# Kernel optimization log

Measured on AMD Instinct MI355X. Metric: run time of the kernel, lower is better.

## Reference

```python
import jax, jax.numpy as jnp
import numpy as np

IN_FEATURES = 4096
OUT_FEATURES = 11008
BATCH = 256


def unpack_i4(q):
    # q: [K//2, N] packed bytes; row 2k = low nibble, row 2k+1 = high nibble
    low = q & 15
    high = (q >> 4) & 15
    # interleave -> [K, N]
    return jnp.stack([low, high], axis=1).reshape(q.shape[0] * 2, q.shape[1])


def setup_inputs() -> dict:
    key = jax.random.key(0)
    k1, k2, k3, k4 = jax.random.split(key, 4)
    x = jax.random.normal(k1, (BATCH, IN_FEATURES), dtype=jnp.float32)
    qweight = jax.random.randint(k2, (IN_FEATURES // 2, OUT_FEATURES), 0, 256, dtype=jnp.int32)
    scales = jax.random.uniform(k3, (OUT_FEATURES,), dtype=jnp.float32)
    zeroes = jax.random.normal(k4, (OUT_FEATURES,), dtype=jnp.float32)
    return {"x": x, "qweight": qweight, "scales": scales, "zeroes": zeroes}


def reference(x, qweight, scales, zeroes):
    # Dequantize: per-output-channel scale/zero over unpacked int4 weights
    w = scales[None, :] * unpack_i4(qweight).astype(jnp.float32) - zeroes[None, :]  # [K, N]
    return x @ w  # [B, N]
```

## Files before the change

kernel.cpp:

```cpp
#include <hip/hip_runtime.h>
#include <stdint.h>

#define K_DIM 4096
#define N_DIM 11008
#define M_DIM 256

typedef uint32_t u32;
using frag_ab = __attribute__((ext_vector_type(8))) short;
using frag_cd = __attribute__((ext_vector_type(4))) float;

typedef __attribute__((address_space(3))) const char lds_cc;

#define DSR128(dst, addr, off)                                       \
    asm volatile("ds_read_b128 %0, %1 offset:" #off                  \
                 : "=&v"(dst) : "v"(addr))
#define DSR32(dst, addr, off)                                        \
    asm volatile("ds_read_b32 %0, %1 offset:" #off                   \
                 : "=&v"(dst) : "v"(addr))
#define LGKM(n) do { asm volatile("s_waitcnt lgkmcnt(" #n ")" ::: "memory"); \
                     __builtin_amdgcn_sched_barrier(0); } while (0)

__device__ __forceinline__ u32 f2bf_rn(float f) {
    u32 u = __builtin_bit_cast(u32, f);
    return (u + 0x7FFFu + ((u >> 16) & 1u)) >> 16;
}
__device__ __forceinline__ float bf2f(u32 b) {
    return __builtin_bit_cast(float, b << 16);
}
__device__ __forceinline__ void gll16(const void* g, void* l) {
    __builtin_amdgcn_global_load_lds(
        (const __attribute__((address_space(1))) u32*)g,
        (__attribute__((address_space(3))) u32*)l, 16, 0, 0);
}

#define BFCVT(q) ((u32)((__mul24((int)(q), 0x4004) & 0x003C003C) | 0x42004200))

__global__ __launch_bounds__(256) void prep_kernel(const float* __restrict__ x,
                                                   ushort* __restrict__ xbf,
                                                   float* __restrict__ rowsum) {
    const int row = blockIdx.x;
    const int tid = threadIdx.x;
    const float* xr = x + (size_t)row * K_DIM;
    ushort* br = xbf + (size_t)row * K_DIM;
    float s = 0.0f;
#pragma unroll
    for (int p = 0; p < 4; ++p) {
        int i = p * 1024 + tid * 4;
        float4 v = *reinterpret_cast<const float4*>(xr + i);
        u32 b0 = f2bf_rn(v.x), b1 = f2bf_rn(v.y), b2 = f2bf_rn(v.z), b3 = f2bf_rn(v.w);
        uint2 o;
        o.x = b0 | (b1 << 16);
        o.y = b2 | (b3 << 16);
        *reinterpret_cast<uint2*>(br + i) = o;
        s += bf2f(b0) + bf2f(b1) + bf2f(b2) + bf2f(b3);
    }
#pragma unroll
    for (int off = 32; off > 0; off >>= 1) s += __shfl_down(s, off, 64);
    __shared__ float wsum[4];
    if ((tid & 63) == 0) wsum[tid >> 6] = s;
    __syncthreads();
    if (tid == 0) rowsum[row] = wsum[0] + wsum[1] + wsum[2] + wsum[3];
}

__global__ __launch_bounds__(256, 3) void gemm_kernel(const int* __restrict__ qw,
                                                      const float* __restrict__ scales,
                                                      const float* __restrict__ zeroes,
                                                      const ushort* __restrict__ xbf,
                                                      const float* __restrict__ rowsum,
                                                      float* __restrict__ out,
                                                      ushort* __restrict__ partial,
                                                      int split4) {
    __shared__ uint4 Alds[3][512];
    __shared__ u32   Blds[3][2048];

    const u32* qwu = (const u32*)qw;
    const int tid  = threadIdx.x;
    const int lane = tid & 63;
    const int wid  = tid >> 6;
    const int l4   = lane & 15;
    const int c    = lane >> 4;

    const int orig = blockIdx.x;
    int nb, mb, sp, NTt;
    if (split4) {
        int wg = (orig & 7) * 86 + (orig >> 3);
        nb = wg >> 3; sp = (wg >> 1) & 3; mb = wg & 1; NTt = 32;
    } else {
        nb = orig >> 1; mb = orig & 1; sp = 0; NTt = 128;
    }
    const int n0 = nb * 128;
    const int m0 = mb * 128;
    const int wm = wid >> 1;
    const int wn = wid & 1;

    const ushort* asrc[2];
#pragma unroll
    for (int j = 0; j < 2; ++j)
        asrc[j] = xbf + (size_t)(m0 + j * 64 + wid * 16 + (lane >> 2)) * K_DIM +
                  sp * 1024 + 8 * ((lane & 3) ^ ((lane >> 3) & 3));
    const u32* bsrc[2];
#pragma unroll
    for (int r = 0; r < 2; ++r)
        bsrc[r] = qwu + (size_t)(sp * 512 + r * 8 + wid * 2 + (lane >> 5)) * N_DIM +
                  n0 + 4 * ((lane & 31) ^ (((wid >> 1) & 1) << 2));

    const u32 aoff  = (u32)((wm * 64 + l4) * 64 + ((c ^ ((l4 >> 1) & 3)) << 4));
    const u32 b0off = (u32)((c * 4) * 512 + (wn * 64 + ((c & 1) << 4) + l4) * 4);
    const u32 b1off = (u32)((c * 4) * 512 + (wn * 64 + ((1 ^ (c & 1)) << 4) + l4) * 4);

    frag_cd acc[4][4];
#pragma unroll
    for (int i = 0; i < 4; ++i)
#pragma unroll
        for (int j = 0; j < 4; ++j)
            acc[i][j] = (frag_cd){0.f, 0.f, 0.f, 0.f};

    auto stage = [&](int t, int buf) {
#pragma unroll
        for (int j = 0; j < 2; ++j)
            gll16(asrc[j] + (size_t)t * 32, &Alds[buf][j * 256 + wid * 64]);
#pragma unroll
        for (int r = 0; r < 2; ++r)
            gll16(bsrc[r] + (size_t)t * 16 * N_DIM, &Blds[buf][r * 1024 + wid * 256]);
    };

    auto compute = [&](int buf) {
        lds_cc* Ab = (lds_cc*)&Alds[buf][0];
        lds_cc* Bb = (lds_cc*)&Blds[buf][0];
        frag_ab afr[4];
        DSR128(afr[0], Ab + aoff, 0);
        DSR128(afr[1], Ab + aoff, 1024);
        DSR128(afr[2], Ab + aoff, 2048);
        DSR128(afr[3], Ab + aoff, 3072);
        u32 bq[16];
        DSR32(bq[0],  Bb + b0off, 0);
        DSR32(bq[1],  Bb + b0off, 512);
        DSR32(bq[2],  Bb + b0off, 1024);
        DSR32(bq[3],  Bb + b0off, 1536);
        DSR32(bq[4],  Bb + b1off, 0);
        DSR32(bq[5],  Bb + b1off, 512);
        DSR32(bq[6],  Bb + b1off, 1024);
        DSR32(bq[7],  Bb + b1off, 1536);
        DSR32(bq[8],  Bb + b0off, 128);
        DSR32(bq[9],  Bb + b0off, 640);
        DSR32(bq[10], Bb + b0off, 1152);
        DSR32(bq[11], Bb + b0off, 1664);
        DSR32(bq[12], Bb + b1off, 128);
        DSR32(bq[13], Bb + b1off, 640);
        DSR32(bq[14], Bb + b1off, 1152);
        DSR32(bq[15], Bb + b1off, 1664);
        LGKM(12);
#pragma unroll
        for (int nf = 0; nf < 4; ++nf) {
            union { frag_ab f; u32 u[4]; } bb;
            bb.u[0] = BFCVT(bq[nf * 4 + 0]);
            bb.u[1] = BFCVT(bq[nf * 4 + 1]);
            bb.u[2] = BFCVT(bq[nf * 4 + 2]);
            bb.u[3] = BFCVT(bq[nf * 4 + 3]);
#pragma unroll
            for (int mf = 0; mf < 4; ++mf)
                acc[mf][nf] = __builtin_amdgcn_mfma_f32_16x16x32_bf16(
                    afr[mf], bb.f, acc[mf][nf], 0, 0, 0);
            if (nf == 0)      LGKM(8);
            else if (nf == 1) LGKM(4);
            else if (nf == 2) LGKM(0);
        }
    };

    stage(0, 0);
    stage(1, 1);

    int cur = 0;
    for (int t = 0; t < NTt; ++t) {
        int pbuf = cur + 2; if (pbuf >= 3) pbuf -= 3;
        if (t + 2 < NTt) {
            stage(t + 2, pbuf);
            asm volatile("s_waitcnt vmcnt(8)" ::: "memory");
        } else if (t + 1 < NTt) {
            asm volatile("s_waitcnt vmcnt(4)" ::: "memory");
        } else {
            asm volatile("s_waitcnt vmcnt(0)" ::: "memory");
        }
        __builtin_amdgcn_s_barrier();
        __builtin_amdgcn_sched_barrier(0);
        compute(cur);
        asm volatile("" ::: "memory");
        __builtin_amdgcn_s_barrier();
        ++cur; if (cur >= 3) cur -= 3;
    }

    float sc[4], zp[4];
#pragma unroll
    for (int nf = 0; nf < 4; ++nf) {
        int n = n0 + wn * 64 + nf * 16 + l4;
        sc[nf] = scales[n];
        zp[nf] = zeroes[n] + 32.0f * sc[nf];
    }
    if (sp == 0) {
        float rs[4][4];
#pragma unroll
        for (int mf = 0; mf < 4; ++mf)
#pragma unroll
            for (int j = 0; j < 4; ++j)
                rs[mf][j] = rowsum[m0 + wm * 64 + mf * 16 + c * 4 + j];
#pragma unroll
        for (int mf = 0; mf < 4; ++mf)
#pragma unroll
            for (int nf = 0; nf < 4; ++nf)
#pragma unroll
                for (int j = 0; j < 4; ++j) {
                    int m = m0 + wm * 64 + mf * 16 + c * 4 + j;
                    out[(size_t)m * N_DIM + n0 + wn * 64 + nf * 16 + l4] =
                        sc[nf] * acc[mf][nf][j] - zp[nf] * rs[mf][j];
                }
    } else {
        ushort* pb = partial + (size_t)(sp - 1) * M_DIM * N_DIM;
#pragma unroll
        for (int mf = 0; mf < 4; ++mf)
#pragma unroll
            for (int nf = 0; nf < 4; ++nf)
#pragma unroll
                for (int j = 0; j < 4; ++j) {
                    int m = m0 + wm * 64 + mf * 16 + c * 4 + j;
                    pb[(size_t)m * N_DIM + n0 + wn * 64 + nf * 16 + l4] =
                        (ushort)f2bf_rn(sc[nf] * acc[mf][nf][j]);
                }
    }
}

__global__ __launch_bounds__(256) void reduce_kernel(float* __restrict__ out,
                                                     const ushort* __restrict__ partial) {
    const size_t NTOT = (size_t)M_DIM * N_DIM;
    size_t i = ((size_t)blockIdx.x * 256 + threadIdx.x) * 4;
    float4 o = *reinterpret_cast<float4*>(out + i);
    ushort4 a = *reinterpret_cast<const ushort4*>(partial + i);
    ushort4 b = *reinterpret_cast<const ushort4*>(partial + NTOT + i);
    ushort4 d = *reinterpret_cast<const ushort4*>(partial + 2 * NTOT + i);
    o.x += bf2f(a.x) + bf2f(b.x) + bf2f(d.x);
    o.y += bf2f(a.y) + bf2f(b.y) + bf2f(d.y);
    o.z += bf2f(a.z) + bf2f(b.z) + bf2f(d.z);
    o.w += bf2f(a.w) + bf2f(b.w) + bf2f(d.w);
    *reinterpret_cast<float4*>(out + i) = o;
}

extern "C" void kernel_launch(void* const* d_in, const int* in_sizes, int n_in,
                              void* d_out, int out_size, void* d_ws, size_t ws_size,
                              hipStream_t stream) {
    const float* x      = (const float*)d_in[0];
    const int*   qw     = (const int*)d_in[1];
    const float* scales = (const float*)d_in[2];
    const float* zeroes = (const float*)d_in[3];
    float* out = (float*)d_out;

    const size_t XBF_BYTES = (size_t)M_DIM * K_DIM * 2;
    const size_t RS_OFF    = XBF_BYTES;
    const size_t P_OFF     = XBF_BYTES + 4096;
    const size_t P_BYTES   = (size_t)3 * M_DIM * N_DIM * 2;

    ushort* xbf    = (ushort*)d_ws;
    float*  rowsum = (float*)((char*)d_ws + RS_OFF);
    ushort* part   = (ushort*)((char*)d_ws + P_OFF);

    const bool split4 = ws_size >= P_OFF + P_BYTES;

    prep_kernel<<<M_DIM, 256, 0, stream>>>(x, xbf, rowsum);
    if (split4) {
        gemm_kernel<<<688, 256, 0, stream>>>(qw, scales, zeroes, xbf, rowsum,
                                             out, part, 1);
        reduce_kernel<<<(M_DIM * N_DIM) / (256 * 4), 256, 0, stream>>>(out, part);
    } else {
        gemm_kernel<<<172, 256, 0, stream>>>(qw, scales, zeroes, xbf, rowsum,
                                             out, nullptr, 0);
    }
}
```

Measured before the change: 50.56 us.

## Double K tile to 64 with two-stage double buffering instead of triple

Doubles the K depth per pipeline stage (64 instead of 32) and switches from a three-buffer to a two-buffer LDS pipeline, halving the number of loop iterations and barrier pairs. The A-tile swizzle is changed to an 8-way XOR pattern to suit the wider 128-byte rows. Launch bounds drop from 3 to 2 blocks per CU because LDS per block grows, which trades occupancy and prefetch depth for less synchronisation overhead.

```diff
diff --git a/kernel.cpp b/kernel.cpp
--- a/kernel.cpp
+++ b/kernel.cpp
@@ -19,6 +19,7 @@
                  : "=&v"(dst) : "v"(addr))
 #define LGKM(n) do { asm volatile("s_waitcnt lgkmcnt(" #n ")" ::: "memory"); \
                      __builtin_amdgcn_sched_barrier(0); } while (0)
+#define VMW(n) asm volatile("s_waitcnt vmcnt(" #n ")" ::: "memory")
 
 __device__ __forceinline__ u32 f2bf_rn(float f) {
     u32 u = __builtin_bit_cast(u32, f);
@@ -62,7 +63,7 @@
     if (tid == 0) rowsum[row] = wsum[0] + wsum[1] + wsum[2] + wsum[3];
 }
 
-__global__ __launch_bounds__(256, 3) void gemm_kernel(const int* __restrict__ qw,
+__global__ __launch_bounds__(256, 2) void gemm_kernel(const int* __restrict__ qw,
                                                       const float* __restrict__ scales,
                                                       const float* __restrict__ zeroes,
                                                       const ushort* __restrict__ xbf,
@@ -70,8 +71,8 @@
                                                       float* __restrict__ out,
                                                       ushort* __restrict__ partial,
                                                       int split4) {
-    __shared__ uint4 Alds[3][512];
-    __shared__ u32   Blds[3][2048];
+    __shared__ uint4 Alds[2][1024];
+    __shared__ u32   Blds[2][4096];
 
     const u32* qwu = (const u32*)qw;
     const int tid  = threadIdx.x;
@@ -84,29 +85,30 @@
     int nb, mb, sp, NTt;
     if (split4) {
         int wg = (orig & 7) * 86 + (orig >> 3);
-        nb = wg >> 3; sp = (wg >> 1) & 3; mb = wg & 1; NTt = 32;
+        nb = wg >> 3; sp = (wg >> 1) & 3; mb = wg & 1; NTt = 16;
     } else {
-        nb = orig >> 1; mb = orig & 1; sp = 0; NTt = 128;
+        nb = orig >> 1; mb = orig & 1; sp = 0; NTt = 64;
     }
     const int n0 = nb * 128;
     const int m0 = mb * 128;
     const int wm = wid >> 1;
     const int wn = wid & 1;
 
-    const ushort* asrc[2];
-#pragma unroll
-    for (int j = 0; j < 2; ++j)
-        asrc[j] = xbf + (size_t)(m0 + j * 64 + wid * 16 + (lane >> 2)) * K_DIM +
-                  sp * 1024 + 8 * ((lane & 3) ^ ((lane >> 3) & 3));
-    const u32* bsrc[2];
-#pragma unroll
-    for (int r = 0; r < 2; ++r)
+    const ushort* asrc[4];
+#pragma unroll
+    for (int j = 0; j < 4; ++j)
+        asrc[j] = xbf + (size_t)(m0 + j * 32 + wid * 8 + (lane >> 3)) * K_DIM +
+                  sp * 1024 + ((lane & 7) ^ (lane >> 3)) * 8;
+    const u32* bsrc[4];
+#pragma unroll
+    for (int r = 0; r < 4; ++r)
         bsrc[r] = qwu + (size_t)(sp * 512 + r * 8 + wid * 2 + (lane >> 5)) * N_DIM +
                   n0 + 4 * ((lane & 31) ^ (((wid >> 1) & 1) << 2));
 
-    const u32 aoff  = (u32)((wm * 64 + l4) * 64 + ((c ^ ((l4 >> 1) & 3)) << 4));
+    const u32 aoff0 = (u32)((wm * 64 + l4) * 128 + (((0 + c) ^ (l4 & 7)) << 4));
+    const u32 aoff1 = (u32)((wm * 64 + l4) * 128 + (((4 + c) ^ (l4 & 7)) << 4));
     const u32 b0off = (u32)((c * 4) * 512 + (wn * 64 + ((c & 1) << 4) + l4) * 4);
-    const u32 b1off = (u32)((c * 4) * 512 + (wn * 64 + ((1 ^ (c & 1)) << 4) + l4) * 4);
+    const u32 b1off = (u32)((c * 4) * 512 + (wn * 64 + (((c & 1) ^ 1) << 4) + l4) * 4);
 
     frag_cd acc[4][4];
 #pragma unroll
@@ -117,76 +119,69 @@
 
     auto stage = [&](int t, int buf) {
 #pragma unroll
-        for (int j = 0; j < 2; ++j)
-            gll16(asrc[j] + (size_t)t * 32, &Alds[buf][j * 256 + wid * 64]);
-#pragma unroll
-        for (int r = 0; r < 2; ++r)
-            gll16(bsrc[r] + (size_t)t * 16 * N_DIM, &Blds[buf][r * 1024 + wid * 256]);
+        for (int j = 0; j < 4; ++j)
+            gll16(asrc[j] + (size_t)t * 64, &Alds[buf][j * 256 + wid * 64]);
+#pragma unroll
+        for (int r = 0; r < 4; ++r)
+            gll16(bsrc[r] + (size_t)t * 32 * N_DIM, &Blds[buf][r * 1024 + wid * 256]);
     };
+
+#define KSTEP(AOFF, I0, I1, I2, I3, I4, I5, I6, I7, I8, I9, Ia, Ib, Ic, Id, Ie, If) { \
+        frag_ab afr[4];                                                      \
+        DSR128(afr[0], Ab + AOFF, 0);                                        \
+        DSR128(afr[1], Ab + AOFF, 2048);                                     \
+        DSR128(afr[2], Ab + AOFF, 4096);                                     \
+        DSR128(afr[3], Ab + AOFF, 6144);                                     \
+        u32 bq[16];                                                          \
+        DSR32(bq[0],  Bb + b0off, I0);  DSR32(bq[1],  Bb + b0off, I1);       \
+        DSR32(bq[2],  Bb + b0off, I2);  DSR32(bq[3],  Bb + b0off, I3);       \
+        DSR32(bq[4],  Bb + b1off, I4);  DSR32(bq[5],  Bb + b1off, I5);       \
+        DSR32(bq[6],  Bb + b1off, I6);  DSR32(bq[7],  Bb + b1off, I7);       \
+        DSR32(bq[8],  Bb + b0off, I8);  DSR32(bq[9],  Bb + b0off, I9);       \
+        DSR32(bq[10], Bb + b0off, Ia);  DSR32(bq[11], Bb + b0off, Ib);       \
+        DSR32(bq[12], Bb + b1off, Ic);  DSR32(bq[13], Bb + b1off, Id);       \
+        DSR32(bq[14], Bb + b1off, Ie);  DSR32(bq[15], Bb + b1off, If);       \
+        LGKM(12);                                                            \
+        _Pragma("unroll")                                                    \
+        for (int nf = 0; nf < 4; ++nf) {                                     \
+            union { frag_ab f; u32 u[4]; } bb;                               \
+            bb.u[0] = BFCVT(bq[nf * 4 + 0]);                                 \
+            bb.u[1] = BFCVT(bq[nf * 4 + 1]);                                 \
+            bb.u[2] = BFCVT(bq[nf * 4 + 2]);                                 \
+            bb.u[3] = BFCVT(bq[nf * 4 + 3]);                                 \
+            _Pragma("unroll")                                                \
+            for (int mf = 0; mf < 4; ++mf)                                   \
+                acc[mf][nf] = __builtin_amdgcn_mfma_f32_16x16x32_bf16(       \
+                    afr[mf], bb.f, acc[mf][nf], 0, 0, 0);                    \
+            if (nf == 0)      LGKM(8);                                       \
+            else if (nf == 1) LGKM(4);                                       \
+            else if (nf == 2) LGKM(0);                                       \
+        } }
 
     auto compute = [&](int buf) {
         lds_cc* Ab = (lds_cc*)&Alds[buf][0];
         lds_cc* Bb = (lds_cc*)&Blds[buf][0];
-        frag_ab afr[4];
-        DSR128(afr[0], Ab + aoff, 0);
-        DSR128(afr[1], Ab + aoff, 1024);
-        DSR128(afr[2], Ab + aoff, 2048);
-        DSR128(afr[3], Ab + aoff, 3072);
-        u32 bq[16];
-        DSR32(bq[0],  Bb + b0off, 0);
-        DSR32(bq[1],  Bb + b0off, 512);
-        DSR32(bq[2],  Bb + b0off, 1024);
-        DSR32(bq[3],  Bb + b0off, 1536);
-        DSR32(bq[4],  Bb + b1off, 0);
-        DSR32(bq[5],  Bb + b1off, 512);
-        DSR32(bq[6],  Bb + b1off, 1024);
-        DSR32(bq[7],  Bb + b1off, 1536);
-        DSR32(bq[8],  Bb + b0off, 128);
-        DSR32(bq[9],  Bb + b0off, 640);
-        DSR32(bq[10], Bb + b0off, 1152);
-        DSR32(bq[11], Bb + b0off, 1664);
-        DSR32(bq[12], Bb + b1off, 128);
-        DSR32(bq[13], Bb + b1off, 640);
-        DSR32(bq[14], Bb + b1off, 1152);
-        DSR32(bq[15], Bb + b1off, 1664);
-        LGKM(12);
-#pragma unroll
-        for (int nf = 0; nf < 4; ++nf) {
-            union { frag_ab f; u32 u[4]; } bb;
-            bb.u[0] = BFCVT(bq[nf * 4 + 0]);
-            bb.u[1] = BFCVT(bq[nf * 4 + 1]);
-            bb.u[2] = BFCVT(bq[nf * 4 + 2]);
-            bb.u[3] = BFCVT(bq[nf * 4 + 3]);
-#pragma unroll
-            for (int mf = 0; mf < 4; ++mf)
-                acc[mf][nf] = __builtin_amdgcn_mfma_f32_16x16x32_bf16(
-                    afr[mf], bb.f, acc[mf][nf], 0, 0, 0);
-            if (nf == 0)      LGKM(8);
-            else if (nf == 1) LGKM(4);
-            else if (nf == 2) LGKM(0);
-        }
+        KSTEP(aoff0, 0, 512, 1024, 1536, 0, 512, 1024, 1536,
+              128, 640, 1152, 1664, 128, 640, 1152, 1664)
+        KSTEP(aoff1, 8192, 8704, 9216, 9728, 8192, 8704, 9216, 9728,
+              8320, 8832, 9344, 9856, 8320, 8832, 9344, 9856)
     };
 
     stage(0, 0);
-    stage(1, 1);
-
-    int cur = 0;
+
     for (int t = 0; t < NTt; ++t) {
-        int pbuf = cur + 2; if (pbuf >= 3) pbuf -= 3;
-        if (t + 2 < NTt) {
-            stage(t + 2, pbuf);
-            asm volatile("s_waitcnt vmcnt(8)" ::: "memory");
-        } else if (t + 1 < NTt) {
-            asm volatile("s_waitcnt vmcnt(4)" ::: "memory");
+        int buf = t & 1;
+        if (t + 1 < NTt) {
+            stage(t + 1, buf ^ 1);
+            VMW(8);
         } else {
-            asm volatile("s_waitcnt vmcnt(0)" ::: "memory");
+            VMW(0);
         }
         __builtin_amdgcn_s_barrier();
         __builtin_amdgcn_sched_barrier(0);
-        compute(cur);
+        compute(buf);
         asm volatile("" ::: "memory");
         __builtin_amdgcn_s_barrier();
-        ++cur; if (cur >= 3) cur -= 3;
     }
 
     float sc[4], zp[4];
@@ -226,6 +221,7 @@
                         (ushort)f2bf_rn(sc[nf] * acc[mf][nf][j]);
                 }
     }
+#undef KSTEP
 }
 
 __global__ __launch_bounds__(256) void reduce_kernel(float* __restrict__ out,
```

Result: slower. 52.75 us (+4.3%).
